# Kernel optimization log

Measured on AMD Instinct MI355X. Metric: run time of the kernel, lower is better.

## Reference

```python
import jax, jax.numpy as jnp
import numpy as np
import math

H = 128          # node_dim == hidden_dim
TED = 128        # time_emb_dim
T = 64
BN = 4096


def _mlp(x, w1, b1, w2, b2):
    # 2-layer MLP with SiLU, matching MLP(n_layer=2, act_fn=SiLU)
    return jax.nn.silu(x @ w1 + b1) @ w2 + b2


def _timestep_embedding(t, dim):
    # get_timestep_embedding for possibly-negative relative indices
    half = dim // 2
    freqs = jnp.exp(jnp.arange(half, dtype=jnp.float32) * (-math.log(10000.0) / (half - 1)))
    arg = t.astype(jnp.float32)[:, None] * freqs[None, :]
    return jnp.concatenate([jnp.sin(arg), jnp.cos(arg)], axis=-1)


def setup_inputs() -> dict:
    key = jax.random.key(0)
    ks = jax.random.split(key, 20)
    s = 1.0 / math.sqrt(H)
    d = {
        "x": jax.random.normal(ks[0], (BN, 3, T), jnp.float32),
        "h": jax.random.normal(ks[1], (BN, H, T), jnp.float32),
        "q_w1": jax.random.normal(ks[2], (H, H), jnp.float32) * s,
        "q_b1": jnp.zeros((H,), jnp.float32),
        "q_w2": jax.random.normal(ks[3], (H, H), jnp.float32) * s,
        "q_b2": jnp.zeros((H,), jnp.float32),
        "k_w1": jax.random.normal(ks[4], (H, H), jnp.float32) * s,
        "k_b1": jnp.zeros((H,), jnp.float32),
        "k_w2": jax.random.normal(ks[5], (H, H), jnp.float32) * s,
        "k_b2": jnp.zeros((H,), jnp.float32),
        "v_w1": jax.random.normal(ks[6], (H, H), jnp.float32) * s,
        "v_b1": jnp.zeros((H,), jnp.float32),
        "v_w2": jax.random.normal(ks[7], (H, H), jnp.float32) * s,
        "v_b2": jnp.zeros((H,), jnp.float32),
        "xm_w1": jax.random.normal(ks[8], (H, H), jnp.float32) * s,
        "xm_b1": jnp.zeros((H,), jnp.float32),
        "xm_w2": jax.random.normal(ks[9], (H, 1), jnp.float32) * s,
        "xm_b2": jnp.zeros((1,), jnp.float32),
        "t_w": jax.random.normal(ks[10], (TED, H), jnp.float32) * (1.0 / math.sqrt(TED)),
        "t_b": jnp.zeros((H,), jnp.float32),
    }
    return d


def reference(x, h, q_w1, q_b1, q_w2, q_b2, k_w1, k_b1, k_w2, k_b2,
              v_w1, v_b1, v_w2, v_b2, xm_w1, xm_b1, xm_w2, xm_b2, t_w, t_b):
    Tn = x.shape[-1]
    # relative time embedding E[t, s, :] of shape [T, T, H]
    ti = jnp.arange(Tn)
    rel = (ti[:, None] - ti[None, :]).reshape(-1)
    E = (_timestep_embedding(rel, TED) @ t_w + t_b).reshape(Tn, Tn, -1)

    # merge_time_dim: [N, H, T] -> [N*T, H]  (token order: node-major, time-minor)
    tok = h.transpose(0, 2, 1)                      # [N, T, H]
    q = _mlp(tok, q_w1, q_b1, q_w2, q_b2)           # [N, T, H]
    k = _mlp(tok, k_w1, k_b1, k_w2, k_b2)           # [N, T, H]
    v = _mlp(tok, v_w1, v_b1, v_w2, v_b2)           # [N, T, H]
    vx = _mlp(v, xm_w1, xm_b1, xm_w2, xm_b2)[..., 0]  # [N, T]

    # scores: q . (k_s + E_ts)  -- decomposed, avoids materializing k_ts [N,H,T,T]
    scores = jnp.einsum('nth,nsh->nts', q, k) + jnp.einsum('nth,tsh->nts', q, E)
    alpha = jax.nn.softmax(scores, axis=-1)          # [N, T, S]

    # h update: sum_s alpha * (v_s + E_ts)
    dh = jnp.einsum('nts,nsh->nth', alpha, v) + jnp.einsum('nts,tsh->nth', alpha, E)
    h_out = h + dh.transpose(0, 2, 1)                # [N, H, T]

    # x update: x_t += sum_s alpha[t,s] * vx[s] * (x_t - x_s)
    w = alpha * vx[:, None, :]                       # [N, T, S]
    x_out = x + x * jnp.sum(w, axis=-1)[:, None, :] - jnp.einsum('nts,nds->ndt', w, x)
    return (x_out, h_out)
```

## Files before the change

kernel.cpp:

```cpp
#include <hip/hip_runtime.h>
#include <hip/hip_bf16.h>
#include <math.h>

#define NN 4096

typedef __attribute__((ext_vector_type(8))) short s8v;
typedef __attribute__((ext_vector_type(4))) float f4v;
typedef __attribute__((ext_vector_type(4))) unsigned int u32x4;
typedef __attribute__((ext_vector_type(2))) unsigned int u32x2;
typedef unsigned short u16;

static __device__ __forceinline__ f4v MFMA16(s8v a, s8v b, f4v c) {
  return __builtin_amdgcn_mfma_f32_16x16x32_bf16(a, b, c, 0, 0, 0);
}
static __device__ __forceinline__ u16 f2bf(float f) {
  union { float f; unsigned int u; } v; v.f = f;
  unsigned int r = v.u + 0x7fffu + ((v.u >> 16) & 1u);
  return (u16)(r >> 16);
}
static __device__ __forceinline__ float bf2f(u16 u) {
  union { unsigned int u; float f; } v; v.u = ((unsigned int)u) << 16;
  return v.f;
}
static __device__ __forceinline__ unsigned int cvt2u(float lo, float hi) {
  __hip_bfloat162 h = __float22bfloat162_rn(make_float2(lo, hi));
  union { __hip_bfloat162 b; unsigned int u; } c; c.b = h; return c.u;
}

#define SW(row, byte)  ((row) * 256 + ((byte) ^ (((row) & 7) << 4)))
#define SWH(row, byte) ((row) * 128 + ((byte) ^ (((row) & 7) << 4)))

#define FA_OFF 0
#define FB_OFF 49152
#define FC_OFF 98304
#define FD_OFF 131072

__global__ void prep_kernel(const float* __restrict__ qw1, const float* __restrict__ kw1,
                            const float* __restrict__ vw1, const float* __restrict__ qw2,
                            const float* __restrict__ kw2, const float* __restrict__ vw2,
                            const float* __restrict__ xmw1,
                            const float* __restrict__ t_w, const float* __restrict__ t_b,
                            u16* __restrict__ wsb) {
  const int b = blockIdx.x, tid = threadIdx.x;
  const int kt = tid >> 6, l = tid & 63, lr = l & 15, lk = l >> 4;
  if (b < 56) {
    const float* W; int mt; u16* base;
    if (b < 24)      { base = wsb + FA_OFF; mt = b;      W = (b < 8) ? qw1 : (b < 16) ? kw1 : vw1; }
    else if (b < 48) { base = wsb + FB_OFF; mt = b - 24; W = (mt < 8) ? qw2 : (mt < 16) ? kw2 : vw2; }
    else             { base = wsb + FC_OFF; mt = b - 48; W = xmw1; }
    const int ch = (mt & 7) * 16;
    u16 o[8];
#pragma unroll
    for (int j = 0; j < 8; ++j) o[j] = f2bf(W[(kt * 32 + lk * 8 + j) * 128 + ch + lr]);
    u32x4 pk;
#pragma unroll
    for (int i = 0; i < 4; ++i) pk[i] = (unsigned int)o[2 * i] | ((unsigned int)o[2 * i + 1] << 16);
    *(u32x4*)&base[((mt * 4 + kt) * 64 + l) * 8] = pk;
  } else {
    const int rt = b - 56;
    const int r = rt * 16 + lr;
    const float rel = (float)(r - 63);
    const int h0 = kt * 32 + lk * 8;
    float acc[8];
#pragma unroll
    for (int j = 0; j < 8; ++j) acc[j] = t_b[h0 + j];
    const float C = -logf(10000.0f) / 63.0f;
    for (int i = 0; i < 64; ++i) {
      float f = expf((float)i * C);
      float a = rel * f;
      float sn = sinf(a), cs = cosf(a);
#pragma unroll
      for (int j = 0; j < 8; ++j) acc[j] = fmaf(sn, t_w[i * 128 + h0 + j], acc[j]);
#pragma unroll
      for (int j = 0; j < 8; ++j) acc[j] = fmaf(cs, t_w[(i + 64) * 128 + h0 + j], acc[j]);
    }
    u16 o[8];
#pragma unroll
    for (int j = 0; j < 8; ++j) o[j] = f2bf(acc[j]);
    u32x4 pk;
#pragma unroll
    for (int i = 0; i < 4; ++i) pk[i] = (unsigned int)o[2 * i] | ((unsigned int)o[2 * i + 1] << 16);
    *(u32x4*)&wsb[FC_OFF + (((8 + rt) * 4 + kt) * 64 + l) * 8] = pk;
    const int ct = h0 >> 4, lrp = h0 & 15;
    const int ktp = r >> 5, lkp = (r >> 3) & 3, jp = r & 7;
#pragma unroll
    for (int j = 0; j < 8; ++j)
      wsb[FD_OFF + ((ct * 4 + ktp) * 64 + lkp * 16 + lrp + j) * 8 + jp] = o[j];
  }
}

template <bool SILU, bool HASB>
__device__ __forceinline__ void tile_gemm(const u16* __restrict__ fr,
                                          const unsigned char* Bl, unsigned char* Ol,
                                          const float* __restrict__ bias,
                                          int ocol, int l) {
  const int lr = l & 15, lk = l >> 4;
  s8v a[4];
#pragma unroll
  for (int kt = 0; kt < 4; ++kt) a[kt] = *(const s8v*)&fr[(kt * 64 + l) * 8];
  float bj[4];
#pragma unroll
  for (int j = 0; j < 4; ++j) bj[j] = HASB ? bias[lk * 4 + j] : 0.f;
  f4v acc[4];
#pragma unroll
  for (int ni = 0; ni < 4; ++ni)
#pragma unroll
    for (int j = 0; j < 4; ++j) acc[ni][j] = bj[j];
#pragma unroll
  for (int kt = 0; kt < 4; ++kt)
#pragma unroll
    for (int ni = 0; ni < 4; ++ni)
      acc[ni] = MFMA16(a[kt], *(const s8v*)(Bl + SW(ni * 16 + lr, kt * 64 + lk * 16)), acc[ni]);
#pragma unroll
  for (int ni = 0; ni < 4; ++ni) {
    int t = ni * 16 + lr;
    float v0 = acc[ni][0], v1 = acc[ni][1], v2 = acc[ni][2], v3 = acc[ni][3];
    if (SILU) {
      v0 *= __builtin_amdgcn_rcpf(1.0f + __expf(-v0));
      v1 *= __builtin_amdgcn_rcpf(1.0f + __expf(-v1));
      v2 *= __builtin_amdgcn_rcpf(1.0f + __expf(-v2));
      v3 *= __builtin_amdgcn_rcpf(1.0f + __expf(-v3));
    }
    u32x2 st; st[0] = cvt2u(v0, v1); st[1] = cvt2u(v2, v3);
    *(u32x2*)(Ol + SW(t, ocol + lk * 8)) = st;
  }
}

__launch_bounds__(512, 4)
__global__ void et_main(const float* __restrict__ xg, const float* __restrict__ hg,
                        const u16* __restrict__ wsb,
                        const float* __restrict__ qb1, const float* __restrict__ qb2,
                        const float* __restrict__ kb1, const float* __restrict__ kb2,
                        const float* __restrict__ vb1, const float* __restrict__ vb2,
                        const float* __restrict__ xmb1, const float* __restrict__ xmw2,
                        const float* __restrict__ xmb2,
                        float* __restrict__ xout, float* __restrict__ hout) {
  __shared__ __align__(16) unsigned char smem[81920];
  unsigned char* S0 = smem;
  unsigned char* S1 = smem + 16384;
  unsigned char* S2 = smem + 32768;
  unsigned char* S3 = smem + 49152;
  unsigned char* S4 = smem + 65536;
  unsigned char* ALP = S0;
  unsigned char* YB  = S0 + 8192;
  float* VXP = (float*)(S0 + 10240);
  float* XLS = (float*)(S0 + 12288);

  const u16* FA = wsb + FA_OFF;
  const u16* FB = wsb + FB_OFF;
  const u16* FC = wsb + FC_OFF;
  const u16* FD = wsb + FD_OFF;

  const int tid = threadIdx.x;
  const int l = tid & 63;
  const int lr = l & 15, lk = l >> 4;
  const int w = __builtin_amdgcn_readfirstlane(tid >> 6);
  const int n = blockIdx.x;
  const size_t hbase = (size_t)n * 8192;

  {
    int t = tid & 63, c0 = (tid >> 6) * 2;
#pragma unroll
    for (int cc = 0; cc < 2; ++cc) {
      int c = c0 + cc;
      float hv[8];
#pragma unroll
      for (int j = 0; j < 8; ++j) hv[j] = hg[hbase + (size_t)(c * 8 + j) * 64 + t];
      u32x4 pk;
#pragma unroll
      for (int j = 0; j < 4; ++j) pk[j] = cvt2u(hv[2 * j], hv[2 * j + 1]);
      *(u32x4*)(S0 + SW(t, c * 16)) = pk;
    }
  }
  __syncthreads();

  tile_gemm<true, true>(FA + (w)      * 2048, S0, S1, qb1 + w * 16, w * 32, l);
  tile_gemm<true, true>(FA + (w + 8)  * 2048, S0, S2, kb1 + w * 16, w * 32, l);
  tile_gemm<true, true>(FA + (w + 16) * 2048, S0, S3, vb1 + w * 16, w * 32, l);
  __syncthreads();

  tile_gemm<false, true>(FB + (w)     * 2048, S1, S4, qb2 + w * 16, w * 32, l);
  tile_gemm<false, true>(FB + (w + 8) * 2048, S2, S0, kb2 + w * 16, w * 32, l);
  __syncthreads();

  tile_gemm<false, true >(FB + (w + 16) * 2048, S3, S1, vb2 + w * 16, w * 32, l);
  tile_gemm<false, false>(FC + (w + 8)  * 2048, S4, S2, nullptr,      w * 32, l);
  __syncthreads();

  float vxr[4];
  {
    const u16* fx = FC + w * 2048;
    s8v a[4];
#pragma unroll
    for (int kt = 0; kt < 4; ++kt) a[kt] = *(const s8v*)&fx[(kt * 64 + l) * 8];
    float bj[4], w2[4];
#pragma unroll
    for (int j = 0; j < 4; ++j) { bj[j] = xmb1[w * 16 + lk * 4 + j]; w2[j] = xmw2[w * 16 + lk * 4 + j]; }
    f4v acc[4];
#pragma unroll
    for (int ni = 0; ni < 4; ++ni)
#pragma unroll
      for (int j = 0; j < 4; ++j) acc[ni][j] = bj[j];
#pragma unroll
    for (int kt = 0; kt < 4; ++kt)
#pragma unroll
      for (int ni = 0; ni < 4; ++ni)
        acc[ni] = MFMA16(a[kt], *(const s8v*)(S1 + SW(ni * 16 + lr, kt * 64 + lk * 16)), acc[ni]);
#pragma unroll
    for (int ni = 0; ni < 4; ++ni) {
      float s = 0.f;
#pragma unroll
      for (int j = 0; j < 4; ++j) {
        float v = acc[ni][j];
        v *= __builtin_amdgcn_rcpf(1.0f + __expf(-v));
        s = fmaf(v, w2[j], s);
      }
      s += __shfl_xor(s, 16, 64);
      s += __shfl_xor(s, 32, 64);
      vxr[ni] = s;
    }
  }
  {
    const int m0 = (w & 3) * 16, n0 = (w >> 2) * 32;
    f4v acc[2];
#pragma unroll
    for (int ni = 0; ni < 2; ++ni)
#pragma unroll
      for (int j = 0; j < 4; ++j) acc[ni][j] = 0.f;
#pragma unroll
    for (int kt = 0; kt < 4; ++kt) {
      s8v a = *(const s8v*)(S0 + SW(m0 + lr, kt * 64 + lk * 16));
#pragma unroll
      for (int ni = 0; ni < 2; ++ni)
        acc[ni] = MFMA16(a, *(const s8v*)(S4 + SW(n0 + ni * 16 + lr, kt * 64 + lk * 16)), acc[ni]);
    }
#pragma unroll
    for (int ni = 0; ni < 2; ++ni) {
      int t = n0 + ni * 16 + lr;
      float4 out;
      float* op = (float*)&out;
#pragma unroll
      for (int j = 0; j < 4; ++j) {
        int s = m0 + lk * 4 + j;
        op[j] = acc[ni][j] + bf2f(*(const u16*)(S2 + SW(t, (t - s + 63) * 2)));
      }
      *(float4*)(S3 + SW(t, m0 * 4 + lk * 16)) = out;
    }
  }
  __syncthreads();

  unsigned int ac[4];
  {
    int t = tid >> 3, g = tid & 7;
    float4 v0 = *(float4*)(S3 + SW(t, g * 32));
    float4 v1 = *(float4*)(S3 + SW(t, g * 32 + 16));
    float e[8] = {v0.x, v0.y, v0.z, v0.w, v1.x, v1.y, v1.z, v1.w};
    float m = e[0];
#pragma unroll
    for (int i = 1; i < 8; ++i) m = fmaxf(m, e[i]);
    m = fmaxf(m, __shfl_xor(m, 1, 64));
    m = fmaxf(m, __shfl_xor(m, 2, 64));
    m = fmaxf(m, __shfl_xor(m, 4, 64));
    float s = 0.f;
#pragma unroll
    for (int i = 0; i < 8; ++i) { e[i] = __expf(e[i] - m); s += e[i]; }
    s += __shfl_xor(s, 1, 64);
    s += __shfl_xor(s, 2, 64);
    s += __shfl_xor(s, 4, 64);
    float inv = __builtin_amdgcn_rcpf(s);
#pragma unroll
    for (int i = 0; i < 4; ++i) ac[i] = cvt2u(e[2 * i] * inv, e[2 * i + 1] * inv);
    u32x4 st; st[0] = ac[0]; st[1] = ac[1]; st[2] = ac[2]; st[3] = ac[3];
    *(u32x4*)(ALP + SWH(t, g * 16)) = st;
    u32x4 zz; zz[0] = zz[1] = zz[2] = zz[3] = 0;
    *(u32x4*)(S4 + tid * 16) = zz;
    *(u32x4*)(S4 + 8192 + tid * 16) = zz;
    if (tid < 96) *(u32x4*)(YB + 512 + tid * 16) = zz;
    if (l < 16) {
#pragma unroll
      for (int ni = 0; ni < 4; ++ni) VXP[w * 64 + ni * 16 + l] = vxr[ni];
    }
    if (tid < 192) XLS[tid] = xg[n * 192 + tid];
  }
  __syncthreads();

  {
    int t = tid >> 3, g = tid & 7;
    u16 ab[8];
#pragma unroll
    for (int i = 0; i < 4; ++i) { ab[2 * i] = (u16)(ac[i] & 0xffffu); ab[2 * i + 1] = (u16)(ac[i] >> 16); }
#pragma unroll
    for (int i = 0; i < 8; ++i)
      *(u16*)(S4 + SW(t, (t + 63 - 8 * g - i) * 2)) = ab[i];
  }
  {
    int c = ((w & 1) << 6) + l;
    int t0 = (w >> 1) << 4;
    u16 vt[16];
#pragma unroll
    for (int i = 0; i < 16; ++i) vt[i] = *(const u16*)(S1 + SW(t0 + i, c * 2));
    u32x4 p0, p1;
#pragma unroll
    for (int i = 0; i < 4; ++i) {
      p0[i] = (unsigned int)vt[2 * i]     | ((unsigned int)vt[2 * i + 1] << 16);
      p1[i] = (unsigned int)vt[8 + 2 * i] | ((unsigned int)vt[9 + 2 * i] << 16);
    }
    *(u32x4*)(S2 + SWH(c, t0 * 2))      = p0;
    *(u32x4*)(S2 + SWH(c, t0 * 2 + 16)) = p1;
  }
  if (tid < 64) {
    float s = VXP[tid];
#pragma unroll
    for (int wv = 1; wv < 8; ++wv) s += VXP[wv * 64 + tid];
    s += xmb2[0];
    unsigned int p0 = cvt2u(s, s * XLS[tid]);
    unsigned int p1 = cvt2u(s * XLS[64 + tid], s * XLS[128 + tid]);
    *(u16*)(YB + SWH(0, 2 * tid)) = (u16)(p0 & 0xffffu);
    *(u16*)(YB + SWH(1, 2 * tid)) = (u16)(p0 >> 16);
    *(u16*)(YB + SWH(2, 2 * tid)) = (u16)(p1 & 0xffffu);
    *(u16*)(YB + SWH(3, 2 * tid)) = (u16)(p1 >> 16);
  }
  __syncthreads();

  {
    const int m0 = w * 16;
    float hld[16];
#pragma unroll
    for (int ni = 0; ni < 4; ++ni) {
      size_t base = hbase + (size_t)(m0 + lk * 4) * 64 + ni * 16 + lr;
#pragma unroll
      for (int j = 0; j < 4; ++j) hld[ni * 4 + j] = hg[base + j * 64];
    }
    f4v acc[4];
#pragma unroll
    for (int ni = 0; ni < 4; ++ni)
#pragma unroll
      for (int j = 0; j < 4; ++j) acc[ni][j] = 0.f;
#pragma unroll
    for (int kt = 0; kt < 2; ++kt) {
      s8v a = *(const s8v*)(S2 + SWH(m0 + lr, kt * 64 + lk * 16));
#pragma unroll
      for (int ni = 0; ni < 4; ++ni)
        acc[ni] = MFMA16(a, *(const s8v*)(ALP + SWH(ni * 16 + lr, kt * 64 + lk * 16)), acc[ni]);
    }
    const u16* fd = FD + w * 2048;
#pragma unroll
    for (int kt = 0; kt < 4; ++kt) {
      s8v a = *(const s8v*)&fd[(kt * 64 + l) * 8];
#pragma unroll
      for (int ni = 0; ni < 4; ++ni)
        acc[ni] = MFMA16(a, *(const s8v*)(S4 + SW(ni * 16 + lr, kt * 64 + lk * 16)), acc[ni]);
    }
#pragma unroll
    for (int ni = 0; ni < 4; ++ni) {
      size_t base = hbase + (size_t)(m0 + lk * 4) * 64 + ni * 16 + lr;
#pragma unroll
      for (int j = 0; j < 4; ++j) hout[base + j * 64] = hld[ni * 4 + j] + acc[ni][j];
    }
    if (w < 4) {
      f4v xa;
#pragma unroll
      for (int j = 0; j < 4; ++j) xa[j] = 0.f;
#pragma unroll
      for (int kt = 0; kt < 2; ++kt)
        xa = MFMA16(*(const s8v*)(YB + SWH(lr, kt * 64 + lk * 16)),
                    *(const s8v*)(ALP + SWH(w * 16 + lr, kt * 64 + lk * 16)), xa);
      if (lk == 0) {
        int t = w * 16 + lr;
        float a1 = xa[0];
#pragma unroll
        for (int d = 0; d < 3; ++d) {
          float xv = XLS[d * 64 + t];
          xout[n * 192 + d * 64 + t] = fmaf(xv, a1, xv) - xa[1 + d];
        }
      }
    }
  }
}

extern "C" void kernel_launch(void* const* d_in, const int* in_sizes, int n_in,
                              void* d_out, int out_size, void* d_ws, size_t ws_size,
                              hipStream_t stream) {
  const float* xg   = (const float*)d_in[0];
  const float* hg   = (const float*)d_in[1];
  const float* qw1  = (const float*)d_in[2];
  const float* qb1  = (const float*)d_in[3];
  const float* qw2  = (const float*)d_in[4];
  const float* qb2  = (const float*)d_in[5];
  const float* kw1  = (const float*)d_in[6];
  const float* kb1  = (const float*)d_in[7];
  const float* kw2  = (const float*)d_in[8];
  const float* kb2  = (const float*)d_in[9];
  const float* vw1  = (const float*)d_in[10];
  const float* vb1  = (const float*)d_in[11];
  const float* vw2  = (const float*)d_in[12];
  const float* vb2  = (const float*)d_in[13];
  const float* xmw1 = (const float*)d_in[14];
  const float* xmb1 = (const float*)d_in[15];
  const float* xmw2 = (const float*)d_in[16];
  const float* xmb2 = (const float*)d_in[17];
  const float* t_w  = (const float*)d_in[18];
  const float* t_b  = (const float*)d_in[19];

  u16* wsb = (u16*)d_ws;
  float* xout = (float*)d_out;
  float* hout = xout + (size_t)NN * 192;

  prep_kernel<<<64, 256, 0, stream>>>(qw1, kw1, vw1, qw2, kw2, vw2, xmw1, t_w, t_b, wsb);
  et_main<<<NN, 512, 0, stream>>>(xg, hg, wsb,
                                  qb1, qb2, kb1, kb2, vb1, vb2, xmb1, xmw2, xmb2,
                                  xout, hout);
}
```

Measured before the change: 174.6 us.

## Restructure attention stage: fuse q·E banded scatter, keep scores in registers, cut a barrier

```diff
diff --git a/kernel.cpp b/kernel.cpp
--- a/kernel.cpp
+++ b/kernel.cpp
@@ -28,7 +28,6 @@
 }
 
 #define SW(row, byte)  ((row) * 256 + ((byte) ^ (((row) & 7) << 4)))
-#define SWH(row, byte) ((row) * 128 + ((byte) ^ (((row) & 7) << 4)))
 
 #define FA_OFF 0
 #define FB_OFF 49152
@@ -93,8 +92,8 @@
 __device__ __forceinline__ void tile_gemm(const u16* __restrict__ fr,
                                           const unsigned char* Bl, unsigned char* Ol,
                                           const float* __restrict__ bias,
-                                          int ocol, int l) {
-  const int lr = l & 15, lk = l >> 4;
+                                          int ocol, int l, int lr, int lk, int swm,
+                                          const int* rb) {
   s8v a[4];
 #pragma unroll
   for (int kt = 0; kt < 4; ++kt) a[kt] = *(const s8v*)&fr[(kt * 64 + l) * 8];
@@ -110,10 +109,10 @@
   for (int kt = 0; kt < 4; ++kt)
 #pragma unroll
     for (int ni = 0; ni < 4; ++ni)
-      acc[ni] = MFMA16(a[kt], *(const s8v*)(Bl + SW(ni * 16 + lr, kt * 64 + lk * 16)), acc[ni]);
+      acc[ni] = MFMA16(a[kt], *(const s8v*)(Bl + ni * 4096 + rb[kt]), acc[ni]);
+  const int ob = lr * 256 + ((ocol + lk * 8) ^ swm);
 #pragma unroll
   for (int ni = 0; ni < 4; ++ni) {
-    int t = ni * 16 + lr;
     float v0 = acc[ni][0], v1 = acc[ni][1], v2 = acc[ni][2], v3 = acc[ni][3];
     if (SILU) {
       v0 *= __builtin_amdgcn_rcpf(1.0f + __expf(-v0));
@@ -122,7 +121,7 @@
       v3 *= __builtin_amdgcn_rcpf(1.0f + __expf(-v3));
     }
     u32x2 st; st[0] = cvt2u(v0, v1); st[1] = cvt2u(v2, v3);
-    *(u32x2*)(Ol + SW(t, ocol + lk * 8)) = st;
+    *(u32x2*)(Ol + ni * 4096 + ob) = st;
   }
 }
 
@@ -141,10 +140,10 @@
   unsigned char* S2 = smem + 32768;
   unsigned char* S3 = smem + 49152;
   unsigned char* S4 = smem + 65536;
-  unsigned char* ALP = S0;
-  unsigned char* YB  = S0 + 8192;
-  float* VXP = (float*)(S0 + 10240);
-  float* XLS = (float*)(S0 + 12288);
+  unsigned char* ALP = S2;
+  unsigned char* YB  = S2 + 8192;
+  float* XLS = (float*)(S2 + 10240);
+  float* VXP = (float*)(S3 + 8192);
 
   const u16* FA = wsb + FA_OFF;
   const u16* FB = wsb + FB_OFF;
@@ -157,6 +156,12 @@
   const int w = __builtin_amdgcn_readfirstlane(tid >> 6);
   const int n = blockIdx.x;
   const size_t hbase = (size_t)n * 8192;
+  const int swm = (lr & 7) << 4;
+  int rb[4], hrb[2];
+#pragma unroll
+  for (int kt = 0; kt < 4; ++kt) rb[kt] = lr * 256 + ((kt * 64 + lk * 16) ^ swm);
+#pragma unroll
+  for (int kt = 0; kt < 2; ++kt) hrb[kt] = lr * 128 + ((kt * 64 + lk * 16) ^ swm);
 
   {
     int t = tid & 63, c0 = (tid >> 6) * 2;
@@ -174,25 +179,49 @@
   }
   __syncthreads();
 
-  tile_gemm<true, true>(FA + (w)      * 2048, S0, S1, qb1 + w * 16, w * 32, l);
-  tile_gemm<true, true>(FA + (w + 8)  * 2048, S0, S2, kb1 + w * 16, w * 32, l);
-  tile_gemm<true, true>(FA + (w + 16) * 2048, S0, S3, vb1 + w * 16, w * 32, l);
-  __syncthreads();
-
-  tile_gemm<false, true>(FB + (w)     * 2048, S1, S4, qb2 + w * 16, w * 32, l);
-  tile_gemm<false, true>(FB + (w + 8) * 2048, S2, S0, kb2 + w * 16, w * 32, l);
-  __syncthreads();
-
-  tile_gemm<false, true >(FB + (w + 16) * 2048, S3, S1, vb2 + w * 16, w * 32, l);
-  tile_gemm<false, false>(FC + (w + 8)  * 2048, S4, S2, nullptr,      w * 32, l);
-  __syncthreads();
-
-  float vxr[4];
+  tile_gemm<true, true>(FA + (w)      * 2048, S0, S1, qb1 + w * 16, w * 32, l, lr, lk, swm, rb);
+  tile_gemm<true, true>(FA + (w + 8)  * 2048, S0, S2, kb1 + w * 16, w * 32, l, lr, lk, swm, rb);
+  tile_gemm<true, true>(FA + (w + 16) * 2048, S0, S3, vb1 + w * 16, w * 32, l, lr, lk, swm, rb);
+  __syncthreads();
+
+  tile_gemm<false, true>(FB + (w)      * 2048, S1, S4, qb2 + w * 16, w * 32, l, lr, lk, swm, rb);
+  tile_gemm<false, true>(FB + (w + 16) * 2048, S3, S0, vb2 + w * 16, w * 32, l, lr, lk, swm, rb);
+  __syncthreads();
+
+  tile_gemm<false, true>(FB + (w + 8) * 2048, S2, S1, kb2 + w * 16, w * 32, l, lr, lk, swm, rb);
   {
-    const u16* fx = FC + w * 2048;
+    const u16* fr = FC + (8 + w) * 2048;
     s8v a[4];
 #pragma unroll
-    for (int kt = 0; kt < 4; ++kt) a[kt] = *(const s8v*)&fx[(kt * 64 + l) * 8];
+    for (int kt = 0; kt < 4; ++kt) a[kt] = *(const s8v*)&fr[(kt * 64 + l) * 8];
+    f4v acc[4];
+#pragma unroll
+    for (int ni = 0; ni < 4; ++ni)
+#pragma unroll
+      for (int j = 0; j < 4; ++j) acc[ni][j] = 0.f;
+#pragma unroll
+    for (int kt = 0; kt < 4; ++kt)
+#pragma unroll
+      for (int ni = 0; ni < 4; ++ni)
+        acc[ni] = MFMA16(a[kt], *(const s8v*)(S4 + ni * 4096 + rb[kt]), acc[ni]);
+    const int rbase = w * 16 + lk * 4;
+#pragma unroll
+    for (int ni = 0; ni < 4; ++ni) {
+      int t = ni * 16 + lr;
+      unsigned int p0 = cvt2u(acc[ni][0], acc[ni][1]);
+      unsigned int p1 = cvt2u(acc[ni][2], acc[ni][3]);
+      int i0 = rbase - t;
+      if ((unsigned)(i0 + 0) < 64u) *(u16*)(S3 + t * 128 + ((2 * (i0 + 0)) ^ swm)) = (u16)(p0 & 0xffffu);
+      if ((unsigned)(i0 + 1) < 64u) *(u16*)(S3 + t * 128 + ((2 * (i0 + 1)) ^ swm)) = (u16)(p0 >> 16);
+      if ((unsigned)(i0 + 2) < 64u) *(u16*)(S3 + t * 128 + ((2 * (i0 + 2)) ^ swm)) = (u16)(p1 & 0xffffu);
+      if ((unsigned)(i0 + 3) < 64u) *(u16*)(S3 + t * 128 + ((2 * (i0 + 3)) ^ swm)) = (u16)(p1 >> 16);
+    }
+  }
+  {
+    const u16* fr = FC + w * 2048;
+    s8v a[4];
+#pragma unroll
+    for (int kt = 0; kt < 4; ++kt) a[kt] = *(const s8v*)&fr[(kt * 64 + l) * 8];
     float bj[4], w2[4];
 #pragma unroll
     for (int j = 0; j < 4; ++j) { bj[j] = xmb1[w * 16 + lk * 4 + j]; w2[j] = xmw2[w * 16 + lk * 4 + j]; }
@@ -205,7 +234,7 @@
     for (int kt = 0; kt < 4; ++kt)
 #pragma unroll
       for (int ni = 0; ni < 4; ++ni)
-        acc[ni] = MFMA16(a[kt], *(const s8v*)(S1 + SW(ni * 16 + lr, kt * 64 + lk * 16)), acc[ni]);
+        acc[ni] = MFMA16(a[kt], *(const s8v*)(S0 + ni * 4096 + rb[kt]), acc[ni]);
 #pragma unroll
     for (int ni = 0; ni < 4; ++ni) {
       float s = 0.f;
@@ -217,108 +246,108 @@
       }
       s += __shfl_xor(s, 16, 64);
       s += __shfl_xor(s, 32, 64);
-      vxr[ni] = s;
-    }
-  }
-  {
-    const int m0 = (w & 3) * 16, n0 = (w >> 2) * 32;
-    f4v acc[2];
-#pragma unroll
-    for (int ni = 0; ni < 2; ++ni)
-#pragma unroll
-      for (int j = 0; j < 4; ++j) acc[ni][j] = 0.f;
-#pragma unroll
-    for (int kt = 0; kt < 4; ++kt) {
-      s8v a = *(const s8v*)(S0 + SW(m0 + lr, kt * 64 + lk * 16));
-#pragma unroll
-      for (int ni = 0; ni < 2; ++ni)
-        acc[ni] = MFMA16(a, *(const s8v*)(S4 + SW(n0 + ni * 16 + lr, kt * 64 + lk * 16)), acc[ni]);
-    }
-#pragma unroll
-    for (int ni = 0; ni < 2; ++ni) {
-      int t = n0 + ni * 16 + lr;
-      float4 out;
-      float* op = (float*)&out;
-#pragma unroll
-      for (int j = 0; j < 4; ++j) {
-        int s = m0 + lk * 4 + j;
-        op[j] = acc[ni][j] + bf2f(*(const u16*)(S2 + SW(t, (t - s + 63) * 2)));
-      }
-      *(float4*)(S3 + SW(t, m0 * 4 + lk * 16)) = out;
-    }
-  }
-  __syncthreads();
-
-  unsigned int ac[4];
-  {
-    int t = tid >> 3, g = tid & 7;
-    float4 v0 = *(float4*)(S3 + SW(t, g * 32));
-    float4 v1 = *(float4*)(S3 + SW(t, g * 32 + 16));
-    float e[8] = {v0.x, v0.y, v0.z, v0.w, v1.x, v1.y, v1.z, v1.w};
-    float m = e[0];
-#pragma unroll
-    for (int i = 1; i < 8; ++i) m = fmaxf(m, e[i]);
-    m = fmaxf(m, __shfl_xor(m, 1, 64));
-    m = fmaxf(m, __shfl_xor(m, 2, 64));
-    m = fmaxf(m, __shfl_xor(m, 4, 64));
+      if (l < 16) VXP[w * 64 + ni * 16 + l] = s;
+    }
+  }
+  __syncthreads();
+
+  unsigned int apk[8];
+  if (w < 4) {
+    const int n0 = w * 16, t = n0 + lr;
+    s8v bq[4];
+#pragma unroll
+    for (int kt = 0; kt < 4; ++kt) bq[kt] = *(const s8v*)(S4 + n0 * 256 + rb[kt]);
+    f4v acc[4];
+#pragma unroll
+    for (int mi = 0; mi < 4; ++mi)
+#pragma unroll
+      for (int j = 0; j < 4; ++j) acc[mi][j] = 0.f;
+#pragma unroll
+    for (int kt = 0; kt < 4; ++kt)
+#pragma unroll
+      for (int mi = 0; mi < 4; ++mi)
+        acc[mi] = MFMA16(*(const s8v*)(S1 + mi * 4096 + rb[kt]), bq[kt], acc[mi]);
+    float e[4][4];
+#pragma unroll
+    for (int mi = 0; mi < 4; ++mi) {
+      u32x2 qv = *(const u32x2*)(S3 + t * 128 + ((120 - 32 * mi - 8 * lk) ^ swm));
+      e[mi][3] = acc[mi][3] + bf2f((u16)(qv[0] & 0xffffu));
+      e[mi][2] = acc[mi][2] + bf2f((u16)(qv[0] >> 16));
+      e[mi][1] = acc[mi][1] + bf2f((u16)(qv[1] & 0xffffu));
+      e[mi][0] = acc[mi][0] + bf2f((u16)(qv[1] >> 16));
+    }
+    float m = e[0][0];
+#pragma unroll
+    for (int mi = 0; mi < 4; ++mi)
+#pragma unroll
+      for (int j = 0; j < 4; ++j) m = fmaxf(m, e[mi][j]);
+    m = fmaxf(m, __shfl_xor(m, 16, 64));
+    m = fmaxf(m, __shfl_xor(m, 32, 64));
     float s = 0.f;
 #pragma unroll
-    for (int i = 0; i < 8; ++i) { e[i] = __expf(e[i] - m); s += e[i]; }
-    s += __shfl_xor(s, 1, 64);
-    s += __shfl_xor(s, 2, 64);
-    s += __shfl_xor(s, 4, 64);
+    for (int mi = 0; mi < 4; ++mi)
+#pragma unroll
+      for (int j = 0; j < 4; ++j) { e[mi][j] = __expf(e[mi][j] - m); s += e[mi][j]; }
+    s += __shfl_xor(s, 16, 64);
+    s += __shfl_xor(s, 32, 64);
     float inv = __builtin_amdgcn_rcpf(s);
 #pragma unroll
-    for (int i = 0; i < 4; ++i) ac[i] = cvt2u(e[2 * i] * inv, e[2 * i + 1] * inv);
-    u32x4 st; st[0] = ac[0]; st[1] = ac[1]; st[2] = ac[2]; st[3] = ac[3];
-    *(u32x4*)(ALP + SWH(t, g * 16)) = st;
+    for (int mi = 0; mi < 4; ++mi) {
+      apk[2 * mi]     = cvt2u(e[mi][0] * inv, e[mi][1] * inv);
+      apk[2 * mi + 1] = cvt2u(e[mi][2] * inv, e[mi][3] * inv);
+      u32x2 st; st[0] = apk[2 * mi]; st[1] = apk[2 * mi + 1];
+      *(u32x2*)(ALP + t * 128 + ((mi * 32 + lk * 8) ^ swm)) = st;
+    }
+  } else if (w == 4) {
+    int t = l;
+    float vx = xmb2[0];
+#pragma unroll
+    for (int wv = 0; wv < 8; ++wv) vx += VXP[wv * 64 + t];
+    float x0 = xg[n * 192 + t], x1 = xg[n * 192 + 64 + t], x2 = xg[n * 192 + 128 + t];
+    XLS[t] = x0; XLS[64 + t] = x1; XLS[128 + t] = x2;
+    unsigned int p0 = cvt2u(vx, vx * x0), p1 = cvt2u(vx * x1, vx * x2);
+    *(u16*)(YB + 0   + ((2 * t) ^ 0))  = (u16)(p0 & 0xffffu);
+    *(u16*)(YB + 128 + ((2 * t) ^ 16)) = (u16)(p0 >> 16);
+    *(u16*)(YB + 256 + ((2 * t) ^ 32)) = (u16)(p1 & 0xffffu);
+    *(u16*)(YB + 384 + ((2 * t) ^ 48)) = (u16)(p1 >> 16);
+  } else if (w == 5) {
     u32x4 zz; zz[0] = zz[1] = zz[2] = zz[3] = 0;
-    *(u32x4*)(S4 + tid * 16) = zz;
-    *(u32x4*)(S4 + 8192 + tid * 16) = zz;
-    if (tid < 96) *(u32x4*)(YB + 512 + tid * 16) = zz;
-    if (l < 16) {
-#pragma unroll
-      for (int ni = 0; ni < 4; ++ni) VXP[w * 64 + ni * 16 + l] = vxr[ni];
-    }
-    if (tid < 192) XLS[tid] = xg[n * 192 + tid];
-  }
-  __syncthreads();
-
-  {
-    int t = tid >> 3, g = tid & 7;
-    u16 ab[8];
-#pragma unroll
-    for (int i = 0; i < 4; ++i) { ab[2 * i] = (u16)(ac[i] & 0xffffu); ab[2 * i + 1] = (u16)(ac[i] >> 16); }
-#pragma unroll
-    for (int i = 0; i < 8; ++i)
-      *(u16*)(S4 + SW(t, (t + 63 - 8 * g - i) * 2)) = ab[i];
-  }
-  {
-    int c = ((w & 1) << 6) + l;
-    int t0 = (w >> 1) << 4;
-    u16 vt[16];
-#pragma unroll
-    for (int i = 0; i < 16; ++i) vt[i] = *(const u16*)(S1 + SW(t0 + i, c * 2));
-    u32x4 p0, p1;
-#pragma unroll
-    for (int i = 0; i < 4; ++i) {
-      p0[i] = (unsigned int)vt[2 * i]     | ((unsigned int)vt[2 * i + 1] << 16);
-      p1[i] = (unsigned int)vt[8 + 2 * i] | ((unsigned int)vt[9 + 2 * i] << 16);
-    }
-    *(u32x4*)(S2 + SWH(c, t0 * 2))      = p0;
-    *(u32x4*)(S2 + SWH(c, t0 * 2 + 16)) = p1;
-  }
-  if (tid < 64) {
-    float s = VXP[tid];
-#pragma unroll
-    for (int wv = 1; wv < 8; ++wv) s += VXP[wv * 64 + tid];
-    s += xmb2[0];
-    unsigned int p0 = cvt2u(s, s * XLS[tid]);
-    unsigned int p1 = cvt2u(s * XLS[64 + tid], s * XLS[128 + tid]);
-    *(u16*)(YB + SWH(0, 2 * tid)) = (u16)(p0 & 0xffffu);
-    *(u16*)(YB + SWH(1, 2 * tid)) = (u16)(p0 >> 16);
-    *(u16*)(YB + SWH(2, 2 * tid)) = (u16)(p1 & 0xffffu);
-    *(u16*)(YB + SWH(3, 2 * tid)) = (u16)(p1 >> 16);
+    *(u32x4*)(YB + 512 + l * 16) = zz;
+    if (l < 32) *(u32x4*)(YB + 1536 + l * 16) = zz;
+  }
+  __syncthreads();
+
+  if (w < 4) {
+    const int n0 = w * 16, t = n0 + lr;
+    u32x4 zz; zz[0] = zz[1] = zz[2] = zz[3] = 0;
+#pragma unroll
+    for (int c = 0; c < 4; ++c) *(u32x4*)(S4 + t * 256 + lk * 64 + c * 16) = zz;
+#pragma unroll
+    for (int mi = 0; mi < 4; ++mi) {
+      int rr = t + 63 - mi * 16 - lk * 4;
+      *(u16*)(S4 + t * 256 + ((2 * (rr - 0)) ^ swm)) = (u16)(apk[2 * mi] & 0xffffu);
+      *(u16*)(S4 + t * 256 + ((2 * (rr - 1)) ^ swm)) = (u16)(apk[2 * mi] >> 16);
+      *(u16*)(S4 + t * 256 + ((2 * (rr - 2)) ^ swm)) = (u16)(apk[2 * mi + 1] & 0xffffu);
+      *(u16*)(S4 + t * 256 + ((2 * (rr - 3)) ^ swm)) = (u16)(apk[2 * mi + 1] >> 16);
+    }
+  } else {
+    const int u = w - 4;
+    const int t0 = (u & 1) * 32;
+    const int c = ((u >> 1) << 6) + l;
+    unsigned int pk[16];
+#pragma unroll
+    for (int i2 = 0; i2 < 16; ++i2) {
+      int t = t0 + 2 * i2;
+      u16 v0 = *(const u16*)(S0 + t * 256 + ((2 * c) ^ ((t & 7) << 4)));
+      u16 v1 = *(const u16*)(S0 + (t + 1) * 256 + ((2 * c) ^ (((t + 1) & 7) << 4)));
+      pk[i2] = (unsigned int)v0 | ((unsigned int)v1 << 16);
+    }
+    const int cm = (c & 7) << 4;
+#pragma unroll
+    for (int cc = 0; cc < 4; ++cc) {
+      u32x4 st; st[0] = pk[4 * cc]; st[1] = pk[4 * cc + 1]; st[2] = pk[4 * cc + 2]; st[3] = pk[4 * cc + 3];
+      *(u32x4*)(S3 + c * 128 + ((t0 * 2 + cc * 16) ^ cm)) = st;
+    }
   }
   __syncthreads();
 
@@ -338,10 +367,10 @@
       for (int j = 0; j < 4; ++j) acc[ni][j] = 0.f;
 #pragma unroll
     for (int kt = 0; kt < 2; ++kt) {
-      s8v a = *(const s8v*)(S2 + SWH(m0 + lr, kt * 64 + lk * 16));
+      s8v a = *(const s8v*)(S3 + w * 2048 + hrb[kt]);
 #pragma unroll
       for (int ni = 0; ni < 4; ++ni)
-        acc[ni] = MFMA16(a, *(const s8v*)(ALP + SWH(ni * 16 + lr, kt * 64 + lk * 16)), acc[ni]);
+        acc[ni] = MFMA16(a, *(const s8v*)(ALP + ni * 2048 + hrb[kt]), acc[ni]);
     }
     const u16* fd = FD + w * 2048;
 #pragma unroll
@@ -349,7 +378,7 @@
       s8v a = *(const s8v*)&fd[(kt * 64 + l) * 8];
 #pragma unroll
       for (int ni = 0; ni < 4; ++ni)
-        acc[ni] = MFMA16(a, *(const s8v*)(S4 + SW(ni * 16 + lr, kt * 64 + lk * 16)), acc[ni]);
+        acc[ni] = MFMA16(a, *(const s8v*)(S4 + ni * 4096 + rb[kt]), acc[ni]);
     }
 #pragma unroll
     for (int ni = 0; ni < 4; ++ni) {
@@ -363,8 +392,8 @@
       for (int j = 0; j < 4; ++j) xa[j] = 0.f;
 #pragma unroll
       for (int kt = 0; kt < 2; ++kt)
-        xa = MFMA16(*(const s8v*)(YB + SWH(lr, kt * 64 + lk * 16)),
-                    *(const s8v*)(ALP + SWH(w * 16 + lr, kt * 64 + lk * 16)), xa);
+        xa = MFMA16(*(const s8v*)(YB + hrb[kt]),
+                    *(const s8v*)(ALP + w * 2048 + hrb[kt]), xa);
       if (lk == 0) {
         int t = w * 16 + lr;
         float a1 = xa[0];
```

After: 175.8 us. About the same (+0.7%).
